# Performance work log

Hardware: AMD Instinct MI355X
Metric: run time of the kernel (lower is better)

Reference implementation:

```python
import jax, jax.numpy as jnp
import numpy as np

NEG = -1e9


def setup_inputs() -> dict:
    key = jax.random.key(0)
    kq, kk, kv, ke = jax.random.split(key, 4)
    B, H, S, D = 4, 16, 2048, 64
    q = jax.random.normal(kq, (B, H, S, D), dtype=jnp.float32)
    k = jax.random.normal(kk, (B, H, S, D), dtype=jnp.float32)
    v = jax.random.normal(kv, (B, H, S, D), dtype=jnp.float32)
    event_length = jax.random.randint(ke, (B,), 0, S, dtype=jnp.int32)
    return {"q": q, "k": k, "v": v, "event_length": event_length}


def reference(q, k, v, event_length):
    B, H, S, D = q.shape
    scale = jnp.sqrt(jnp.asarray(D, dtype=jnp.float32))
    # [b,h,s,q] scores
    scores = jnp.einsum('bhsd,bhqd->bhsq', q, k) / scale
    idx = jnp.arange(S)
    el = event_length[:, None]  # [B,1]
    valid = idx[None, :] < el   # [B,S]
    # mask[b,s,q] = valid[b,s] & valid[b,q]; broadcast over heads
    mask = (valid[:, None, :, None] & valid[:, None, None, :])  # [B,1,S,S]
    scores = jnp.where(mask, scores, NEG)
    attn = jax.nn.softmax(scores, axis=-1)
    # dropout p=0.0 (eval): identity
    out = jnp.einsum('bhsq,bhqd->bhsd', attn, v)
    return out
```

## Files before the change

### kernel.cpp

```cpp
#include <hip/hip_runtime.h>
#include <hip/hip_bf16.h>


#define SQ 2048
#define DH 64
#define NBH 64
#define TK 64
#define NTILE 32
#define TILE_B 8192
#define LDE 72
#define LVP 68

typedef __attribute__((ext_vector_type(4))) float f32x4;
typedef __attribute__((ext_vector_type(8))) short bf16x8;
typedef __attribute__((ext_vector_type(4))) unsigned int u32x4;
typedef __attribute__((ext_vector_type(2))) unsigned int u32x2;

__device__ __forceinline__ unsigned int pk2(float lo, float hi) {
    __hip_bfloat162 h = __float22bfloat162_rn(float2{lo, hi});
    union { __hip_bfloat162 h; unsigned int u; } c; c.h = h;
    return c.u;
}

__device__ __forceinline__ float bfu16_to_f(unsigned short s) {
    union { unsigned int u; float f; } c; c.u = ((unsigned int)s) << 16;
    return c.f;
}

__device__ __forceinline__ void async_cp16(const void* g, void* l) {
    __builtin_amdgcn_global_load_lds(
        (const __attribute__((address_space(1))) unsigned int*)g,
        (__attribute__((address_space(3))) unsigned int*)l, 16, 0, 0);
}


__global__ __launch_bounds__(256)
void convkv(const float* __restrict__ K, const float* __restrict__ V,
            const int* __restrict__ EL, float* __restrict__ MV,
            char* __restrict__ Kbt, char* __restrict__ Vbt) {
    const int bh = blockIdx.x >> 5;
    const int kt = blockIdx.x & 31;
    const int k0 = kt * TK;
    const int el = EL[bh >> 4];
    const int t = threadIdx.x;
    const int r  = t >> 2;
    const int dc = t & 3;

    __shared__ short LV[64][LVP];

    {
        const float* vp = V + ((size_t)bh * SQ + k0 + r) * DH + dc * 16;
        f32x4 a = *(const f32x4*)vp;
        f32x4 b = *(const f32x4*)(vp + 4);
        f32x4 c2 = *(const f32x4*)(vp + 8);
        f32x4 d2 = *(const f32x4*)(vp + 12);
        u32x4 w0, w1;
        w0[0] = pk2(a[0], a[1]);  w0[1] = pk2(a[2], a[3]);
        w0[2] = pk2(b[0], b[1]);  w0[3] = pk2(b[2], b[3]);
        w1[0] = pk2(c2[0], c2[1]); w1[1] = pk2(c2[2], c2[3]);
        w1[2] = pk2(d2[0], d2[1]); w1[3] = pk2(d2[2], d2[3]);
        *(u32x4*)&LV[r][dc * 16]     = w0;
        *(u32x4*)&LV[r][dc * 16 + 8] = w1;
    }

    if (k0 < el) {
        const float* kp = K + ((size_t)bh * SQ + k0 + r) * DH + dc * 16;
        f32x4 a = *(const f32x4*)kp;
        f32x4 b = *(const f32x4*)(kp + 4);
        f32x4 c2 = *(const f32x4*)(kp + 8);
        f32x4 d2 = *(const f32x4*)(kp + 12);
        u32x4 w0, w1;
        w0[0] = pk2(a[0], a[1]);  w0[1] = pk2(a[2], a[3]);
        w0[2] = pk2(b[0], b[1]);  w0[3] = pk2(b[2], b[3]);
        w1[0] = pk2(c2[0], c2[1]); w1[1] = pk2(c2[2], c2[3]);
        w1[2] = pk2(d2[0], d2[1]); w1[3] = pk2(d2[2], d2[3]);
        char* kb = Kbt + (size_t)(bh * NTILE + kt) * TILE_B + r * 128;
        *(u32x4*)(kb + (((dc * 2)     ^ (r & 7)) << 4)) = w0;
        *(u32x4*)(kb + (((dc * 2 + 1) ^ (r & 7)) << 4)) = w1;
    }

    __syncthreads();

    const int dd  = t >> 2;
    const int seg = t & 3;
    float msum = 0.f;
    unsigned int wv[8];
    #pragma unroll
    for (int i = 0; i < 8; ++i) {
        const int pos = seg * 16 + 2 * i;
        const int key = (pos & ~31) | ((pos & 4) << 2) | ((pos & 24) >> 1) | (pos & 3);
        const unsigned short s0 = (unsigned short)LV[key][dd];
        const unsigned short s1 = (unsigned short)LV[key + 1][dd];
        msum += bfu16_to_f(s0) + bfu16_to_f(s1);
        wv[i] = (unsigned int)s0 | ((unsigned int)s1 << 16);
    }
    msum += __shfl_xor(msum, 1);
    msum += __shfl_xor(msum, 2);
    if (seg == 0) atomicAdd(&MV[bh * DH + dd], msum * (1.0f / (float)SQ));

    if (k0 < el) {
        char* vb = Vbt + (size_t)(bh * NTILE + kt) * TILE_B + dd * 128;
        u32x4 o0 = {wv[0], wv[1], wv[2], wv[3]};
        u32x4 o1 = {wv[4], wv[5], wv[6], wv[7]};
        *(u32x4*)(vb + (((seg * 2)     ^ (dd & 7)) << 4)) = o0;
        *(u32x4*)(vb + (((seg * 2 + 1) ^ (dd & 7)) << 4)) = o1;
    }
}

__global__ __launch_bounds__(256, 4)
void flash7(const float* __restrict__ Q, const int* __restrict__ EL,
            const float* __restrict__ MV, float* __restrict__ O,
            const char* __restrict__ Kbt, const char* __restrict__ Vbt,
            int* __restrict__ ticket) {
    const int t = threadIdx.x;

    {
        const int bh0 = blockIdx.x & (NBH - 1);
        const int qb0 = (blockIdx.x >> 6) * 128;
        const int elb = EL[bh0 >> 4];
        if (qb0 >= elb) {
            float* Op = O + (size_t)bh0 * SQ * DH;
            const int c16 = t & 15, r0 = t >> 4;
            f32x4 mv = *(const f32x4*)(MV + bh0 * DH + c16 * 4);
            #pragma unroll
            for (int i = 0; i < 8; ++i)
                *(f32x4*)(Op + (size_t)(qb0 + r0 + i * 16) * DH + c16 * 4) = mv;
        }
    }

    const int el0 = EL[0], el1 = EL[1], el2 = EL[2], el3 = EL[3];
    const int v0 = (el0 + 127) >> 7, v1 = (el1 + 127) >> 7;
    const int v2 = (el2 + 127) >> 7, v3 = (el3 + 127) >> 7;
    const int n0 = 16 * v0, n1 = n0 + 16 * v1, n2 = n1 + 16 * v2;
    const int nvalid = n2 + 16 * v3;

    __shared__ short KT[2][TK * DH];
    __shared__ short VT[2][TK * DH];
    __shared__ int item_s;

    const int wq = t >> 6, lane = t & 63, qd = lane >> 4, c = lane & 15;
    const int cs = c & 7;

    for (;;) {
        if (t == 0) item_s = atomicAdd(ticket, 1);
        __syncthreads();
        const int it = item_s;
        if (it >= nvalid) break;

        int b, u, vb, el;
        if      (it < n0) { b = 0; u = it;      vb = v0; el = el0; }
        else if (it < n1) { b = 1; u = it - n0; vb = v1; el = el1; }
        else if (it < n2) { b = 2; u = it - n1; vb = v2; el = el2; }
        else              { b = 3; u = it - n2; vb = v3; el = el3; }
        const int head  = u / vb;
        const int qt    = u - head * vb;
        const int bh    = b * 16 + head;
        const int qbase = qt * 128;

        const float* Qp = Q + (size_t)bh * SQ * DH;
        float*       Op = O + (size_t)bh * SQ * DH;
        const char*  Kt = Kbt + (size_t)bh * NTILE * TILE_B;
        const char*  Vt = Vbt + (size_t)bh * NTILE * TILE_B;

        const float sc = 0.125f * 1.44269504f;
        bf16x8 qf[2][2];
        #pragma unroll
        for (int nt = 0; nt < 2; ++nt) {
            const int row = qbase + wq * 32 + nt * 16 + c;
            #pragma unroll
            for (int kc = 0; kc < 2; ++kc) {
                const float* p = Qp + (size_t)row * DH + kc * 32 + qd * 8;
                f32x4 a  = *(const f32x4*)p;
                f32x4 bq = *(const f32x4*)(p + 4);
                u32x4 f;
                f[0] = pk2(a[0] * sc, a[1] * sc);
                f[1] = pk2(a[2] * sc, a[3] * sc);
                f[2] = pk2(bq[0] * sc, bq[1] * sc);
                f[3] = pk2(bq[2] * sc, bq[3] * sc);
                qf[nt][kc] = *(bf16x8*)&f;
            }
        }

        float l_[2] = {0.f, 0.f};
        f32x4 oacc[4][2];
        #pragma unroll
        for (int dt = 0; dt < 4; ++dt) {
            oacc[dt][0] = (f32x4){0.f, 0.f, 0.f, 0.f};
            oacc[dt][1] = (f32x4){0.f, 0.f, 0.f, 0.f};
        }

        const int nkt = (el + TK - 1) >> 6;

        {
            async_cp16(Kt + (size_t)t * 16,        (char*)&KT[0][0] + wq * 1024);
            async_cp16(Kt + 4096 + (size_t)t * 16, (char*)&KT[0][0] + 4096 + wq * 1024);
            async_cp16(Vt + (size_t)t * 16,        (char*)&VT[0][0] + wq * 1024);
            async_cp16(Vt + 4096 + (size_t)t * 16, (char*)&VT[0][0] + 4096 + wq * 1024);
        }
        asm volatile("s_waitcnt vmcnt(0)" ::: "memory");
        __syncthreads();

        int buf = 0;
        for (int kt = 0; kt < nkt; ++kt) {
            if (kt + 1 < nkt) {
                const char* gK = Kt + (size_t)(kt + 1) * TILE_B + t * 16;
                const char* gV = Vt + (size_t)(kt + 1) * TILE_B + t * 16;
                char* lK = (char*)&KT[buf ^ 1][0] + wq * 1024;
                char* lV = (char*)&VT[buf ^ 1][0] + wq * 1024;
                async_cp16(gK,        lK);
                async_cp16(gK + 4096, lK + 4096);
                async_cp16(gV,        lV);
                async_cp16(gV + 4096, lV + 4096);
            }
            const int k0 = kt * TK;

            const char* Kb = (const char*)&KT[buf][0];
            f32x4 st[4][2];
            #pragma unroll
            for (int mt = 0; mt < 4; ++mt) {
                const char* rp = Kb + (mt * 16 + c) * 128;
                bf16x8 a0 = *(const bf16x8*)(rp + (((qd)     ^ cs) << 4));
                bf16x8 a1 = *(const bf16x8*)(rp + (((qd + 4) ^ cs) << 4));
                #pragma unroll
                for (int nt = 0; nt < 2; ++nt) {
                    f32x4 acc = (f32x4){0.f, 0.f, 0.f, 0.f};
                    acc = __builtin_amdgcn_mfma_f32_16x16x32_bf16(a0, qf[nt][0], acc, 0, 0, 0);
                    acc = __builtin_amdgcn_mfma_f32_16x16x32_bf16(a1, qf[nt][1], acc, 0, 0, 0);
                    st[mt][nt] = acc;
                }
            }

            if (k0 + TK > el) {
                #pragma unroll
                for (int mt = 0; mt < 4; ++mt)
                    #pragma unroll
                    for (int r = 0; r < 4; ++r)
                        if (k0 + mt * 16 + qd * 4 + r >= el) {
                            st[mt][0][r] = -1e30f;
                            st[mt][1][r] = -1e30f;
                        }
            }

            u32x4 pw[2][2];
            #pragma unroll
            for (int nt = 0; nt < 2; ++nt) {
                #pragma unroll
                for (int mt = 0; mt < 4; ++mt) {
                    const float p0 = __builtin_amdgcn_exp2f(st[mt][nt][0]);
                    const float p1 = __builtin_amdgcn_exp2f(st[mt][nt][1]);
                    const float p2 = __builtin_amdgcn_exp2f(st[mt][nt][2]);
                    const float p3 = __builtin_amdgcn_exp2f(st[mt][nt][3]);
                    l_[nt] += (p0 + p1) + (p2 + p3);
                    pw[nt][mt >> 1][(mt & 1) * 2]     = pk2(p0, p1);
                    pw[nt][mt >> 1][(mt & 1) * 2 + 1] = pk2(p2, p3);
                }
            }

            const char* Vb = (const char*)&VT[buf][0];
            #pragma unroll
            for (int kc = 0; kc < 2; ++kc) {
                bf16x8 pb0 = *(bf16x8*)&pw[0][kc];
                bf16x8 pb1 = *(bf16x8*)&pw[1][kc];
                #pragma unroll
                for (int dt = 0; dt < 4; ++dt) {
                    const char* vp = Vb + (dt * 16 + c) * 128 + (((kc * 4 + qd) ^ cs) << 4);
                    bf16x8 vf = *(const bf16x8*)vp;
                    oacc[dt][0] = __builtin_amdgcn_mfma_f32_16x16x32_bf16(vf, pb0, oacc[dt][0], 0, 0, 0);
                    oacc[dt][1] = __builtin_amdgcn_mfma_f32_16x16x32_bf16(vf, pb1, oacc[dt][1], 0, 0, 0);
                }
            }

            asm volatile("s_waitcnt vmcnt(0)" ::: "memory");
            __syncthreads();
            buf ^= 1;
        }

        #pragma unroll
        for (int nt = 0; nt < 2; ++nt) {
            l_[nt] += __shfl_xor(l_[nt], 16);
            l_[nt] += __shfl_xor(l_[nt], 32);
        }

        #pragma unroll
        for (int nt = 0; nt < 2; ++nt) {
            const int qrow = qbase + wq * 32 + nt * 16 + c;
            if (qrow < el) {
                const float inv = 1.0f / l_[nt];
                #pragma unroll
                for (int dt = 0; dt < 4; ++dt) {
                    f32x4 o = oacc[dt][nt];
                    o[0] *= inv; o[1] *= inv; o[2] *= inv; o[3] *= inv;
                    *(f32x4*)(Op + (size_t)qrow * DH + dt * 16 + qd * 4) = o;
                }
            } else {
                #pragma unroll
                for (int dt = 0; dt < 4; ++dt)
                    *(f32x4*)(Op + (size_t)qrow * DH + dt * 16 + qd * 4) =
                        *(const f32x4*)(MV + bh * DH + dt * 16 + qd * 4);
            }
        }
    }
}


__global__ __launch_bounds__(256)
void meanv_k(const float* __restrict__ V, float* __restrict__ MV) {
    const int bh  = blockIdx.x >> 4;
    const int seg = blockIdx.x & 15;
    const float* vp = V + ((size_t)bh * SQ + (size_t)seg * 128) * DH;
    const int c = threadIdx.x & 15;
    const int r = threadIdx.x >> 4;
    const float* p = vp + (size_t)r * DH + c * 4;
    f32x4 s0 = *(const f32x4*)(p);
    f32x4 s1 = *(const f32x4*)(p + 16 * DH);
    f32x4 s2 = *(const f32x4*)(p + 32 * DH);
    f32x4 s3 = *(const f32x4*)(p + 48 * DH);
    s0 += *(const f32x4*)(p + 64 * DH);
    s1 += *(const f32x4*)(p + 80 * DH);
    s2 += *(const f32x4*)(p + 96 * DH);
    s3 += *(const f32x4*)(p + 112 * DH);
    f32x4 s = (s0 + s1) + (s2 + s3);
    __shared__ f32x4 red[16][16];
    red[r][c] = s;
    __syncthreads();
    if (threadIdx.x < 16) {
        f32x4 a = red[0][threadIdx.x];
        #pragma unroll
        for (int j = 1; j < 16; ++j) a += red[j][threadIdx.x];
        const float inv = 1.0f / (float)SQ;
        atomicAdd(&MV[bh * DH + threadIdx.x * 4 + 0], a[0] * inv);
        atomicAdd(&MV[bh * DH + threadIdx.x * 4 + 1], a[1] * inv);
        atomicAdd(&MV[bh * DH + threadIdx.x * 4 + 2], a[2] * inv);
        atomicAdd(&MV[bh * DH + threadIdx.x * 4 + 3], a[3] * inv);
    }
}

__global__ __launch_bounds__(256, 3)
void flash5(const float* __restrict__ Q, const float* __restrict__ K,
            const float* __restrict__ V, const int* __restrict__ EL,
            const float* __restrict__ MV, float* __restrict__ O,
            int* __restrict__ ticket) {
    const int t = threadIdx.x;
    {
        const int bh0    = blockIdx.x & (NBH - 1);
        const int qbase0 = (blockIdx.x >> 6) * 128;
        const int elb    = EL[bh0 >> 4];
        if (qbase0 >= elb) {
            float* Op = O + (size_t)bh0 * SQ * DH;
            const int c16 = t & 15, r0 = t >> 4;
            f32x4 mv = *(const f32x4*)(MV + bh0 * DH + c16 * 4);
            #pragma unroll
            for (int i = 0; i < 8; ++i)
                *(f32x4*)(Op + (size_t)(qbase0 + r0 + i * 16) * DH + c16 * 4) = mv;
        }
    }

    const int el0 = EL[0], el1 = EL[1], el2 = EL[2], el3 = EL[3];
    const int v0 = (el0 + 127) >> 7, v1 = (el1 + 127) >> 7;
    const int v2 = (el2 + 127) >> 7, v3 = (el3 + 127) >> 7;
    const int n0 = 16 * v0, n1 = n0 + 16 * v1, n2 = n1 + 16 * v2;
    const int nvalid = n2 + 16 * v3;

    __shared__ short Kb[TK][LDE];
    __shared__ short Vt[DH][LDE];
    __shared__ short Pl[4][32][LDE];
    __shared__ int item_s;

    const int wq = t >> 6, lane = t & 63, qd = lane >> 4, c = lane & 15;
    const int ksrow = t >> 2;
    const int ksdc  = t & 3;
    const int vpair = t & 31;
    const int vdg   = t >> 5;

    for (;;) {
        if (t == 0) item_s = atomicAdd(ticket, 1);
        __syncthreads();
        const int it = item_s;
        if (it >= nvalid) break;

        int b, u, vb, el;
        if      (it < n0) { b = 0; u = it;      vb = v0; el = el0; }
        else if (it < n1) { b = 1; u = it - n0; vb = v1; el = el1; }
        else if (it < n2) { b = 2; u = it - n1; vb = v2; el = el2; }
        else              { b = 3; u = it - n2; vb = v3; el = el3; }
        const int head  = u / vb;
        const int qt    = u - head * vb;
        const int bh    = b * 16 + head;
        const int qbase = qt * 128;

        const size_t base = (size_t)bh * SQ * DH;
        const float* Qp = Q + base;
        const float* Kp = K + base;
        const float* Vp = V + base;
        float* Op = O + base;

        const float sc = 0.125f * 1.44269504f;
        bf16x8 qf[2][2];
        #pragma unroll
        for (int nt = 0; nt < 2; ++nt) {
            const int row = qbase + wq * 32 + nt * 16 + c;
            #pragma unroll
            for (int kc = 0; kc < 2; ++kc) {
                const float* p = Qp + (size_t)row * DH + kc * 32 + qd * 8;
                f32x4 a  = *(const f32x4*)p;
                f32x4 bb = *(const f32x4*)(p + 4);
                u32x4 f;
                f[0] = pk2(a[0] * sc, a[1] * sc);
                f[1] = pk2(a[2] * sc, a[3] * sc);
                f[2] = pk2(bb[0] * sc, bb[1] * sc);
                f[3] = pk2(bb[2] * sc, bb[3] * sc);
                qf[nt][kc] = *(bf16x8*)&f;
            }
        }

        float l_[2] = {0.f, 0.f};
        f32x4 oacc[4][2];
        #pragma unroll
        for (int dt = 0; dt < 4; ++dt)
            #pragma unroll
            for (int nt = 0; nt < 2; ++nt)
                oacc[dt][nt] = (f32x4){0.f, 0.f, 0.f, 0.f};

        const int nkt = (el + TK - 1) / TK;

        f32x4 kg0, kg1, kg2, kg3, vg0, vg1, vg2, vg3;
        {
            const float* kp = Kp + (size_t)ksrow * DH + ksdc * 16;
            kg0 = *(const f32x4*)kp;
            kg1 = *(const f32x4*)(kp + 4);
            kg2 = *(const f32x4*)(kp + 8);
            kg3 = *(const f32x4*)(kp + 12);
            const float* vp0 = Vp + (size_t)(2 * vpair) * DH + vdg * 8;
            vg0 = *(const f32x4*)vp0;
            vg1 = *(const f32x4*)(vp0 + 4);
            vg2 = *(const f32x4*)(vp0 + DH);
            vg3 = *(const f32x4*)(vp0 + DH + 4);
        }

        for (int kt = 0; kt < nkt; ++kt) {
            const int k0 = kt * TK;

            __syncthreads();
            {
                u32x4 w0, w1;
                w0[0] = pk2(kg0[0], kg0[1]); w0[1] = pk2(kg0[2], kg0[3]);
                w0[2] = pk2(kg1[0], kg1[1]); w0[3] = pk2(kg1[2], kg1[3]);
                w1[0] = pk2(kg2[0], kg2[1]); w1[1] = pk2(kg2[2], kg2[3]);
                w1[2] = pk2(kg3[0], kg3[1]); w1[3] = pk2(kg3[2], kg3[3]);
                *(u32x4*)&Kb[ksrow][ksdc * 16]     = w0;
                *(u32x4*)&Kb[ksrow][ksdc * 16 + 8] = w1;
            }
            {
                #pragma unroll
                for (int i = 0; i < 4; ++i) {
                    *(unsigned int*)&Vt[vdg * 8 + i][2 * vpair]     = pk2(vg0[i], vg2[i]);
                    *(unsigned int*)&Vt[vdg * 8 + 4 + i][2 * vpair] = pk2(vg1[i], vg3[i]);
                }
            }
            __syncthreads();

            if (kt + 1 < nkt) {
                const int kn = k0 + TK;
                const float* kp = Kp + (size_t)(kn + ksrow) * DH + ksdc * 16;
                kg0 = *(const f32x4*)kp;
                kg1 = *(const f32x4*)(kp + 4);
                kg2 = *(const f32x4*)(kp + 8);
                kg3 = *(const f32x4*)(kp + 12);
                const float* vp0 = Vp + (size_t)(kn + 2 * vpair) * DH + vdg * 8;
                vg0 = *(const f32x4*)vp0;
                vg1 = *(const f32x4*)(vp0 + 4);
                vg2 = *(const f32x4*)(vp0 + DH);
                vg3 = *(const f32x4*)(vp0 + DH + 4);
            }

            f32x4 st[4][2];
            #pragma unroll
            for (int mt = 0; mt < 4; ++mt) {
                bf16x8 a0 = *(const bf16x8*)&Kb[mt * 16 + c][qd * 8];
                bf16x8 a1 = *(const bf16x8*)&Kb[mt * 16 + c][32 + qd * 8];
                #pragma unroll
                for (int nt = 0; nt < 2; ++nt) {
                    f32x4 acc = (f32x4){0.f, 0.f, 0.f, 0.f};
                    acc = __builtin_amdgcn_mfma_f32_16x16x32_bf16(a0, qf[nt][0], acc, 0, 0, 0);
                    acc = __builtin_amdgcn_mfma_f32_16x16x32_bf16(a1, qf[nt][1], acc, 0, 0, 0);
                    st[mt][nt] = acc;
                }
            }

            if (k0 + TK > el) {
                #pragma unroll
                for (int mt = 0; mt < 4; ++mt)
                    #pragma unroll
                    for (int r = 0; r < 4; ++r)
                        if (k0 + mt * 16 + qd * 4 + r >= el) {
                            st[mt][0][r] = -1e30f;
                            st[mt][1][r] = -1e30f;
                        }
            }

            #pragma unroll
            for (int nt = 0; nt < 2; ++nt) {
                #pragma unroll
                for (int mt = 0; mt < 4; ++mt) {
                    const float p0 = exp2f(st[mt][nt][0]);
                    const float p1 = exp2f(st[mt][nt][1]);
                    const float p2 = exp2f(st[mt][nt][2]);
                    const float p3 = exp2f(st[mt][nt][3]);
                    l_[nt] += (p0 + p1) + (p2 + p3);
                    u32x2 pw;
                    pw[0] = pk2(p0, p1);
                    pw[1] = pk2(p2, p3);
                    *(u32x2*)&Pl[wq][nt * 16 + c][mt * 16 + qd * 4] = pw;
                }
            }

            #pragma unroll
            for (int kc = 0; kc < 2; ++kc) {
                bf16x8 pb0 = *(const bf16x8*)&Pl[wq][c][kc * 32 + qd * 8];
                bf16x8 pb1 = *(const bf16x8*)&Pl[wq][16 + c][kc * 32 + qd * 8];
                #pragma unroll
                for (int dt = 0; dt < 4; ++dt) {
                    bf16x8 vf = *(const bf16x8*)&Vt[dt * 16 + c][kc * 32 + qd * 8];
                    oacc[dt][0] = __builtin_amdgcn_mfma_f32_16x16x32_bf16(vf, pb0, oacc[dt][0], 0, 0, 0);
                    oacc[dt][1] = __builtin_amdgcn_mfma_f32_16x16x32_bf16(vf, pb1, oacc[dt][1], 0, 0, 0);
                }
            }
        }

        #pragma unroll
        for (int nt = 0; nt < 2; ++nt) {
            l_[nt] += __shfl_xor(l_[nt], 16);
            l_[nt] += __shfl_xor(l_[nt], 32);
        }

        #pragma unroll
        for (int nt = 0; nt < 2; ++nt) {
            const int row = qbase + wq * 32 + nt * 16 + c;
            if (row < el) {
                const float inv = 1.0f / l_[nt];
                #pragma unroll
                for (int dt = 0; dt < 4; ++dt) {
                    f32x4 o = oacc[dt][nt];
                    o[0] *= inv; o[1] *= inv; o[2] *= inv; o[3] *= inv;
                    *(f32x4*)(Op + (size_t)row * DH + dt * 16 + qd * 4) = o;
                }
            } else {
                #pragma unroll
                for (int dt = 0; dt < 4; ++dt) {
                    f32x4 mv = *(const f32x4*)(MV + bh * DH + dt * 16 + qd * 4);
                    *(f32x4*)(Op + (size_t)row * DH + dt * 16 + qd * 4) = mv;
                }
            }
        }
    }
}


extern "C" void kernel_launch(void* const* d_in, const int* in_sizes, int n_in,
                              void* d_out, int out_size, void* d_ws, size_t ws_size,
                              hipStream_t stream) {
    const float* q  = (const float*)d_in[0];
    const float* k  = (const float*)d_in[1];
    const float* v  = (const float*)d_in[2];
    const int*   el = (const int*)d_in[3];
    float* out = (float*)d_out;

    const size_t kbt_bytes = (size_t)NBH * NTILE * TILE_B;
    const size_t needed    = 65536 + 2 * kbt_bytes;

    if (ws_size >= needed) {
        float* mv  = (float*)d_ws;
        int*   tk  = (int*)((char*)d_ws + 16384);
        char*  kbt = (char*)d_ws + 65536;
        char*  vbt = kbt + kbt_bytes;

        hipMemsetAsync(d_ws, 0, 65536, stream);
        convkv<<<dim3(NBH * NTILE), dim3(256), 0, stream>>>(k, v, el, mv, kbt, vbt);
        flash7<<<dim3(NBH * (SQ / 128)), dim3(256), 0, stream>>>(q, el, mv, out, kbt, vbt, tk);
    } else {
        float* mv = (float*)d_ws;
        int*   tk = (int*)((char*)d_ws + NBH * DH * sizeof(float));

        hipMemsetAsync(d_ws, 0, NBH * DH * sizeof(float) + 64, stream);
        meanv_k<<<dim3(NBH * 16), dim3(256), 0, stream>>>(v, mv);
        flash5<<<dim3(NBH * (SQ / 128)), dim3(256), 0, stream>>>(q, k, v, el, mv, out, tk);
    }
}
```

Baseline: 197.2 us.

## Load K/V fragments directly from global in MFMA order, per-wave work items

The convkv pass now writes K and V tiles in an MFMA-fragment-ordered layout, so each lane reads its operands straight from global memory with coalesced 16-byte loads. The double-buffered LDS staging and block-wide barriers in the attention kernel are removed. Work items become 32-row chunks claimed per wave through a per-wave atomic ticket, and occupancy is lowered to 3 blocks per CU to make room for the extra registers holding K/V fragments. The trade is more L2/global traffic, with no LDS sharing across waves and no explicit prefetch, in exchange for finer load balancing and no synchronisation.

New measurement: 210.4 us. 6.7% more time.

```diff
diff --git a/kernel.cpp b/kernel.cpp
--- a/kernel.cpp
+++ b/kernel.cpp
@@ -25,12 +25,6 @@
 __device__ __forceinline__ float bfu16_to_f(unsigned short s) {
     union { unsigned int u; float f; } c; c.u = ((unsigned int)s) << 16;
     return c.f;
-}
-
-__device__ __forceinline__ void async_cp16(const void* g, void* l) {
-    __builtin_amdgcn_global_load_lds(
-        (const __attribute__((address_space(1))) unsigned int*)g,
-        (__attribute__((address_space(3))) unsigned int*)l, 16, 0, 0);
 }
 
 
@@ -74,9 +68,12 @@
         w0[2] = pk2(b[0], b[1]);  w0[3] = pk2(b[2], b[3]);
         w1[0] = pk2(c2[0], c2[1]); w1[1] = pk2(c2[2], c2[3]);
         w1[2] = pk2(d2[0], d2[1]); w1[3] = pk2(d2[2], d2[3]);
-        char* kb = Kbt + (size_t)(bh * NTILE + kt) * TILE_B + r * 128;
-        *(u32x4*)(kb + (((dc * 2)     ^ (r & 7)) << 4)) = w0;
-        *(u32x4*)(kb + (((dc * 2 + 1) ^ (r & 7)) << 4)) = w1;
+        char* kb = Kbt + (size_t)(bh * NTILE + kt) * TILE_B;
+        const int fi  = (r >> 4) * 2 + (dc >> 1);
+        const int qd0 = (dc & 1) * 2;
+        char* d0 = kb + fi * 1024 + qd0 * 256 + (r & 15) * 16;
+        *(u32x4*)d0         = w0;
+        *(u32x4*)(d0 + 256) = w1;
     }
 
     __syncthreads();
@@ -99,16 +96,19 @@
     if (seg == 0) atomicAdd(&MV[bh * DH + dd], msum * (1.0f / (float)SQ));
 
     if (k0 < el) {
-        char* vb = Vbt + (size_t)(bh * NTILE + kt) * TILE_B + dd * 128;
+        char* vbb = Vbt + (size_t)(bh * NTILE + kt) * TILE_B;
+        const int fi  = (seg >> 1) * 4 + (dd >> 4);
+        const int qd0 = (seg & 1) * 2;
+        char* d0 = vbb + fi * 1024 + qd0 * 256 + (dd & 15) * 16;
         u32x4 o0 = {wv[0], wv[1], wv[2], wv[3]};
         u32x4 o1 = {wv[4], wv[5], wv[6], wv[7]};
-        *(u32x4*)(vb + (((seg * 2)     ^ (dd & 7)) << 4)) = o0;
-        *(u32x4*)(vb + (((seg * 2 + 1) ^ (dd & 7)) << 4)) = o1;
-    }
-}
-
-__global__ __launch_bounds__(256, 4)
-void flash7(const float* __restrict__ Q, const int* __restrict__ EL,
+        *(u32x4*)d0         = o0;
+        *(u32x4*)(d0 + 256) = o1;
+    }
+}
+
+__global__ __launch_bounds__(256, 3)
+void flash8(const float* __restrict__ Q, const int* __restrict__ EL,
             const float* __restrict__ MV, float* __restrict__ O,
             const char* __restrict__ Kbt, const char* __restrict__ Vbt,
             int* __restrict__ ticket) {
@@ -117,56 +117,55 @@
     {
         const int bh0 = blockIdx.x & (NBH - 1);
         const int qb0 = (blockIdx.x >> 6) * 128;
-        const int elb = EL[bh0 >> 4];
-        if (qb0 >= elb) {
+        const int el32b = (EL[bh0 >> 4] + 31) & ~31;
+        if (qb0 + 127 >= el32b) {
             float* Op = O + (size_t)bh0 * SQ * DH;
             const int c16 = t & 15, r0 = t >> 4;
             f32x4 mv = *(const f32x4*)(MV + bh0 * DH + c16 * 4);
             #pragma unroll
-            for (int i = 0; i < 8; ++i)
-                *(f32x4*)(Op + (size_t)(qb0 + r0 + i * 16) * DH + c16 * 4) = mv;
+            for (int i = 0; i < 8; ++i) {
+                const int row = qb0 + r0 + i * 16;
+                if (row >= el32b)
+                    *(f32x4*)(Op + (size_t)row * DH + c16 * 4) = mv;
+            }
         }
     }
 
     const int el0 = EL[0], el1 = EL[1], el2 = EL[2], el3 = EL[3];
-    const int v0 = (el0 + 127) >> 7, v1 = (el1 + 127) >> 7;
-    const int v2 = (el2 + 127) >> 7, v3 = (el3 + 127) >> 7;
-    const int n0 = 16 * v0, n1 = n0 + 16 * v1, n2 = n1 + 16 * v2;
-    const int nvalid = n2 + 16 * v3;
-
-    __shared__ short KT[2][TK * DH];
-    __shared__ short VT[2][TK * DH];
-    __shared__ int item_s;
-
-    const int wq = t >> 6, lane = t & 63, qd = lane >> 4, c = lane & 15;
-    const int cs = c & 7;
+    const int w0_ = (el0 + 31) >> 5, w1_ = (el1 + 31) >> 5;
+    const int w2_ = (el2 + 31) >> 5, w3_ = (el3 + 31) >> 5;
+    const int n0 = 16 * w0_, n1 = n0 + 16 * w1_, n2 = n1 + 16 * w2_;
+    const int nvalid = n2 + 16 * w3_;
+
+    const int lane = t & 63, qd = lane >> 4, c = lane & 15;
+    const float sc = 0.125f * 1.44269504f;
 
     for (;;) {
-        if (t == 0) item_s = atomicAdd(ticket, 1);
-        __syncthreads();
-        const int it = item_s;
+        int mytk = 0;
+        if (lane == 0) mytk = atomicAdd(ticket, 1);
+        const int it = __shfl(mytk, 0);
         if (it >= nvalid) break;
 
-        int b, u, vb, el;
-        if      (it < n0) { b = 0; u = it;      vb = v0; el = el0; }
-        else if (it < n1) { b = 1; u = it - n0; vb = v1; el = el1; }
-        else if (it < n2) { b = 2; u = it - n1; vb = v2; el = el2; }
-        else              { b = 3; u = it - n2; vb = v3; el = el3; }
-        const int head  = u / vb;
-        const int qt    = u - head * vb;
+        int b, u, wb, el;
+        if      (it < n0) { b = 0; u = it;      wb = w0_; el = el0; }
+        else if (it < n1) { b = 1; u = it - n0; wb = w1_; el = el1; }
+        else if (it < n2) { b = 2; u = it - n1; wb = w2_; el = el2; }
+        else              { b = 3; u = it - n2; wb = w3_; el = el3; }
+        const int head  = u / wb;
+        const int qt    = u - head * wb;
         const int bh    = b * 16 + head;
-        const int qbase = qt * 128;
+        const int qbase = qt * 32;
 
         const float* Qp = Q + (size_t)bh * SQ * DH;
         float*       Op = O + (size_t)bh * SQ * DH;
-        const char*  Kt = Kbt + (size_t)bh * NTILE * TILE_B;
-        const char*  Vt = Vbt + (size_t)bh * NTILE * TILE_B;
-
-        const float sc = 0.125f * 1.44269504f;
+        const size_t tb = (size_t)bh * NTILE * TILE_B + (size_t)lane * 16;
+        const char*  Kt = Kbt + tb;
+        const char*  Vt = Vbt + tb;
+
         bf16x8 qf[2][2];
         #pragma unroll
         for (int nt = 0; nt < 2; ++nt) {
-            const int row = qbase + wq * 32 + nt * 16 + c;
+            const int row = qbase + nt * 16 + c;
             #pragma unroll
             for (int kc = 0; kc < 2; ++kc) {
                 const float* p = Qp + (size_t)row * DH + kc * 32 + qd * 8;
@@ -191,88 +190,65 @@
 
         const int nkt = (el + TK - 1) >> 6;
 
-        {
-            async_cp16(Kt + (size_t)t * 16,        (char*)&KT[0][0] + wq * 1024);
-            async_cp16(Kt + 4096 + (size_t)t * 16, (char*)&KT[0][0] + 4096 + wq * 1024);
-            async_cp16(Vt + (size_t)t * 16,        (char*)&VT[0][0] + wq * 1024);
-            async_cp16(Vt + 4096 + (size_t)t * 16, (char*)&VT[0][0] + 4096 + wq * 1024);
-        }
-        asm volatile("s_waitcnt vmcnt(0)" ::: "memory");
-        __syncthreads();
-
-        int buf = 0;
         for (int kt = 0; kt < nkt; ++kt) {
-            if (kt + 1 < nkt) {
-                const char* gK = Kt + (size_t)(kt + 1) * TILE_B + t * 16;
-                const char* gV = Vt + (size_t)(kt + 1) * TILE_B + t * 16;
-                char* lK = (char*)&KT[buf ^ 1][0] + wq * 1024;
-                char* lV = (char*)&VT[buf ^ 1][0] + wq * 1024;
-                async_cp16(gK,        lK);
-                async_cp16(gK + 4096, lK + 4096);
-                async_cp16(gV,        lV);
-                async_cp16(gV + 4096, lV + 4096);
-            }
+            const char* kb = Kt + (size_t)kt * TILE_B;
+            const char* vb = Vt + (size_t)kt * TILE_B;
+
+            bf16x8 ka[8];
+            #pragma unroll
+            for (int i = 0; i < 8; ++i)
+                ka[i] = *(const bf16x8*)(kb + i * 1024);
+            bf16x8 va[8];
+            #pragma unroll
+            for (int i = 0; i < 8; ++i)
+                va[i] = *(const bf16x8*)(vb + i * 1024);
+
             const int k0 = kt * TK;
-
-            const char* Kb = (const char*)&KT[buf][0];
-            f32x4 st[4][2];
+            const bool straddle = (k0 + TK > el);
+
+            u32x4 pw[2][2];
             #pragma unroll
             for (int mt = 0; mt < 4; ++mt) {
-                const char* rp = Kb + (mt * 16 + c) * 128;
-                bf16x8 a0 = *(const bf16x8*)(rp + (((qd)     ^ cs) << 4));
-                bf16x8 a1 = *(const bf16x8*)(rp + (((qd + 4) ^ cs) << 4));
-                #pragma unroll
-                for (int nt = 0; nt < 2; ++nt) {
-                    f32x4 acc = (f32x4){0.f, 0.f, 0.f, 0.f};
-                    acc = __builtin_amdgcn_mfma_f32_16x16x32_bf16(a0, qf[nt][0], acc, 0, 0, 0);
-                    acc = __builtin_amdgcn_mfma_f32_16x16x32_bf16(a1, qf[nt][1], acc, 0, 0, 0);
-                    st[mt][nt] = acc;
-                }
-            }
-
-            if (k0 + TK > el) {
-                #pragma unroll
-                for (int mt = 0; mt < 4; ++mt)
+                f32x4 s0 = (f32x4){0.f, 0.f, 0.f, 0.f};
+                s0 = __builtin_amdgcn_mfma_f32_16x16x32_bf16(ka[mt*2],   qf[0][0], s0, 0, 0, 0);
+                s0 = __builtin_amdgcn_mfma_f32_16x16x32_bf16(ka[mt*2+1], qf[0][1], s0, 0, 0, 0);
+                f32x4 s1 = (f32x4){0.f, 0.f, 0.f, 0.f};
+                s1 = __builtin_amdgcn_mfma_f32_16x16x32_bf16(ka[mt*2],   qf[1][0], s1, 0, 0, 0);
+                s1 = __builtin_amdgcn_mfma_f32_16x16x32_bf16(ka[mt*2+1], qf[1][1], s1, 0, 0, 0);
+
+                if (straddle) {
                     #pragma unroll
                     for (int r = 0; r < 4; ++r)
                         if (k0 + mt * 16 + qd * 4 + r >= el) {
-                            st[mt][0][r] = -1e30f;
-                            st[mt][1][r] = -1e30f;
+                            s0[r] = -1e30f;
+                            s1[r] = -1e30f;
                         }
-            }
-
-            u32x4 pw[2][2];
-            #pragma unroll
-            for (int nt = 0; nt < 2; ++nt) {
-                #pragma unroll
-                for (int mt = 0; mt < 4; ++mt) {
-                    const float p0 = __builtin_amdgcn_exp2f(st[mt][nt][0]);
-                    const float p1 = __builtin_amdgcn_exp2f(st[mt][nt][1]);
-                    const float p2 = __builtin_amdgcn_exp2f(st[mt][nt][2]);
-                    const float p3 = __builtin_amdgcn_exp2f(st[mt][nt][3]);
+                }
+
+                #pragma unroll
+                for (int nt = 0; nt < 2; ++nt) {
+                    const f32x4 s = nt ? s1 : s0;
+                    const float p0 = __builtin_amdgcn_exp2f(s[0]);
+                    const float p1 = __builtin_amdgcn_exp2f(s[1]);
+                    const float p2 = __builtin_amdgcn_exp2f(s[2]);
+                    const float p3 = __builtin_amdgcn_exp2f(s[3]);
                     l_[nt] += (p0 + p1) + (p2 + p3);
                     pw[nt][mt >> 1][(mt & 1) * 2]     = pk2(p0, p1);
                     pw[nt][mt >> 1][(mt & 1) * 2 + 1] = pk2(p2, p3);
                 }
             }
 
-            const char* Vb = (const char*)&VT[buf][0];
             #pragma unroll
             for (int kc = 0; kc < 2; ++kc) {
                 bf16x8 pb0 = *(bf16x8*)&pw[0][kc];
                 bf16x8 pb1 = *(bf16x8*)&pw[1][kc];
                 #pragma unroll
                 for (int dt = 0; dt < 4; ++dt) {
-                    const char* vp = Vb + (dt * 16 + c) * 128 + (((kc * 4 + qd) ^ cs) << 4);
-                    bf16x8 vf = *(const bf16x8*)vp;
+                    bf16x8 vf = va[kc * 4 + dt];
                     oacc[dt][0] = __builtin_amdgcn_mfma_f32_16x16x32_bf16(vf, pb0, oacc[dt][0], 0, 0, 0);
                     oacc[dt][1] = __builtin_amdgcn_mfma_f32_16x16x32_bf16(vf, pb1, oacc[dt][1], 0, 0, 0);
                 }
             }
-
-            asm volatile("s_waitcnt vmcnt(0)" ::: "memory");
-            __syncthreads();
-            buf ^= 1;
         }
 
         #pragma unroll
@@ -283,7 +259,7 @@
 
         #pragma unroll
         for (int nt = 0; nt < 2; ++nt) {
-            const int qrow = qbase + wq * 32 + nt * 16 + c;
+            const int qrow = qbase + nt * 16 + c;
             if (qrow < el) {
                 const float inv = 1.0f / l_[nt];
                 #pragma unroll
@@ -576,7 +552,7 @@
 
         hipMemsetAsync(d_ws, 0, 65536, stream);
         convkv<<<dim3(NBH * NTILE), dim3(256), 0, stream>>>(k, v, el, mv, kbt, vbt);
-        flash7<<<dim3(NBH * (SQ / 128)), dim3(256), 0, stream>>>(q, el, mv, out, kbt, vbt, tk);
+        flash8<<<dim3(NBH * (SQ / 128)), dim3(256), 0, stream>>>(q, el, mv, out, kbt, vbt, tk);
     } else {
         float* mv = (float*)d_ws;
         int*   tk = (int*)((char*)d_ws + NBH * DH * sizeof(float));
```

## Triple-buffer K/V tiles, enlarge query blocks, pre-swizzle fragment layout

Applied to the files above, without the earlier changes.

The attention kernel now runs 512-thread blocks that each cover 256 query rows, so every staged K/V tile feeds twice as much work. K/V tiles are prefetched two steps ahead through a three-slot LDS ring, with partial vmcnt waits replacing the full drain at the end of each step. The conversion kernel writes K/V in an MFMA-fragment-ordered layout so LDS reads become plain contiguous lane loads with no XOR swizzle. Work items are split into eight ticket groups with batches sorted by length, and s_setprio is raised around the MFMA sections. LDS use per block grows and the early-exit mean fill loop changes shape, so occupancy and correctness of the fill path are the main risks.

Measured after the change: 193.8 us. No clear change (-1.7%).

```diff
diff --git a/kernel.cpp b/kernel.cpp
--- a/kernel.cpp
+++ b/kernel.cpp
@@ -15,6 +15,8 @@
 typedef __attribute__((ext_vector_type(8))) short bf16x8;
 typedef __attribute__((ext_vector_type(4))) unsigned int u32x4;
 typedef __attribute__((ext_vector_type(2))) unsigned int u32x2;
+
+#define VMCNT(n) asm volatile("s_waitcnt vmcnt(" #n ")" ::: "memory")
 
 __device__ __forceinline__ unsigned int pk2(float lo, float hi) {
     __hip_bfloat162 h = __float22bfloat162_rn(float2{lo, hi});
@@ -74,9 +76,12 @@
         w0[2] = pk2(b[0], b[1]);  w0[3] = pk2(b[2], b[3]);
         w1[0] = pk2(c2[0], c2[1]); w1[1] = pk2(c2[2], c2[3]);
         w1[2] = pk2(d2[0], d2[1]); w1[3] = pk2(d2[2], d2[3]);
-        char* kb = Kbt + (size_t)(bh * NTILE + kt) * TILE_B + r * 128;
-        *(u32x4*)(kb + (((dc * 2)     ^ (r & 7)) << 4)) = w0;
-        *(u32x4*)(kb + (((dc * 2 + 1) ^ (r & 7)) << 4)) = w1;
+        char* kb = Kbt + (size_t)(bh * NTILE + kt) * TILE_B;
+        const int fi  = (r >> 4) * 2 + (dc >> 1);
+        const int qd0 = (dc & 1) * 2;
+        char* d0 = kb + fi * 1024 + qd0 * 256 + (r & 15) * 16;
+        *(u32x4*)d0         = w0;
+        *(u32x4*)(d0 + 256) = w1;
     }
 
     __syncthreads();
@@ -99,24 +104,27 @@
     if (seg == 0) atomicAdd(&MV[bh * DH + dd], msum * (1.0f / (float)SQ));
 
     if (k0 < el) {
-        char* vb = Vbt + (size_t)(bh * NTILE + kt) * TILE_B + dd * 128;
+        char* vbb = Vbt + (size_t)(bh * NTILE + kt) * TILE_B;
+        const int fi  = (seg >> 1) * 4 + (dd >> 4);
+        const int qd0 = (seg & 1) * 2;
+        char* d0 = vbb + fi * 1024 + qd0 * 256 + (dd & 15) * 16;
         u32x4 o0 = {wv[0], wv[1], wv[2], wv[3]};
         u32x4 o1 = {wv[4], wv[5], wv[6], wv[7]};
-        *(u32x4*)(vb + (((seg * 2)     ^ (dd & 7)) << 4)) = o0;
-        *(u32x4*)(vb + (((seg * 2 + 1) ^ (dd & 7)) << 4)) = o1;
-    }
-}
-
-__global__ __launch_bounds__(256, 4)
-void flash7(const float* __restrict__ Q, const int* __restrict__ EL,
-            const float* __restrict__ MV, float* __restrict__ O,
-            const char* __restrict__ Kbt, const char* __restrict__ Vbt,
-            int* __restrict__ ticket) {
+        *(u32x4*)d0         = o0;
+        *(u32x4*)(d0 + 256) = o1;
+    }
+}
+
+__global__ __launch_bounds__(512, 4)
+void flash10(const float* __restrict__ Q, const int* __restrict__ EL,
+             const float* __restrict__ MV, float* __restrict__ O,
+             const char* __restrict__ Kbt, const char* __restrict__ Vbt,
+             int* __restrict__ ticket) {
     const int t = threadIdx.x;
 
     {
         const int bh0 = blockIdx.x & (NBH - 1);
-        const int qb0 = (blockIdx.x >> 6) * 128;
+        const int qb0 = (blockIdx.x >> 6) * 256;
         const int elb = EL[bh0 >> 4];
         if (qb0 >= elb) {
             float* Op = O + (size_t)bh0 * SQ * DH;
@@ -124,45 +132,67 @@
             f32x4 mv = *(const f32x4*)(MV + bh0 * DH + c16 * 4);
             #pragma unroll
             for (int i = 0; i < 8; ++i)
-                *(f32x4*)(Op + (size_t)(qb0 + r0 + i * 16) * DH + c16 * 4) = mv;
-        }
-    }
-
-    const int el0 = EL[0], el1 = EL[1], el2 = EL[2], el3 = EL[3];
-    const int v0 = (el0 + 127) >> 7, v1 = (el1 + 127) >> 7;
-    const int v2 = (el2 + 127) >> 7, v3 = (el3 + 127) >> 7;
-    const int n0 = 16 * v0, n1 = n0 + 16 * v1, n2 = n1 + 16 * v2;
-    const int nvalid = n2 + 16 * v3;
-
-    __shared__ short KT[2][TK * DH];
-    __shared__ short VT[2][TK * DH];
+                *(f32x4*)(Op + (size_t)(qb0 + r0 + i * 32) * DH + c16 * 4) = mv;
+        }
+    }
+
+    int ka0 = EL[0], va0 = 0;
+    int ka1 = EL[1], va1 = 1;
+    int ka2 = EL[2], va2 = 2;
+    int ka3 = EL[3], va3 = 3;
+    #define CSWAP(x, y) if (ka##x < ka##y) { int tk_ = ka##x, tv_ = va##x; \
+        ka##x = ka##y; va##x = va##y; ka##y = tk_; va##y = tv_; }
+    CSWAP(0, 1) CSWAP(2, 3) CSWAP(0, 2) CSWAP(1, 3) CSWAP(1, 2)
+    #undef CSWAP
+    const int c0 = 2 * ((ka0 + 255) >> 8);
+    const int c1 = 2 * ((ka1 + 255) >> 8);
+    const int c2 = 2 * ((ka2 + 255) >> 8);
+    const int c3 = 2 * ((ka3 + 255) >> 8);
+    const int nvalid = c0 + c1 + c2 + c3;
+
+    __shared__ char KB[3 * TILE_B];
+    __shared__ char VB[3 * TILE_B];
     __shared__ int item_s;
 
+    const int grp = blockIdx.x & 7;
     const int wq = t >> 6, lane = t & 63, qd = lane >> 4, c = lane & 15;
-    const int cs = c & 7;
+    const float sc = 0.125f * 1.44269504f;
 
     for (;;) {
-        if (t == 0) item_s = atomicAdd(ticket, 1);
+        if (t == 0) item_s = atomicAdd(&ticket[grp], 1);
         __syncthreads();
         const int it = item_s;
         if (it >= nvalid) break;
 
-        int b, u, vb, el;
-        if      (it < n0) { b = 0; u = it;      vb = v0; el = el0; }
-        else if (it < n1) { b = 1; u = it - n0; vb = v1; el = el1; }
-        else if (it < n2) { b = 2; u = it - n1; vb = v2; el = el2; }
-        else              { b = 3; u = it - n2; vb = v3; el = el3; }
-        const int head  = u / vb;
-        const int qt    = u - head * vb;
-        const int bh    = b * 16 + head;
-        const int qbase = qt * 128;
+        int u = it, b, el;
+        if (u < c0)             { b = va0; el = ka0; }
+        else { u -= c0;
+        if (u < c1)             { b = va1; el = ka1; }
+        else { u -= c1;
+        if (u < c2)             { b = va2; el = ka2; }
+        else { u -= c2;           b = va3; el = ka3; } } }
+        const int vb_ = (el + 255) >> 8;
+        const int hh  = u / vb_;
+        const int qt  = u - hh * vb_;
+        const int bh  = b * 16 + grp + hh * 8;
+        const int qbase = qt * 256;
 
         const float* Qp = Q + (size_t)bh * SQ * DH;
         float*       Op = O + (size_t)bh * SQ * DH;
-        const char*  Kt = Kbt + (size_t)bh * NTILE * TILE_B;
-        const char*  Vt = Vbt + (size_t)bh * NTILE * TILE_B;
-
-        const float sc = 0.125f * 1.44269504f;
+        const char*  Kt = Kbt + (size_t)bh * NTILE * TILE_B + t * 16;
+        const char*  Vt = Vbt + (size_t)bh * NTILE * TILE_B + t * 16;
+        char* const  kdst = KB + wq * 1024;
+        char* const  vdst = VB + wq * 1024;
+
+        const int nkt = (el + TK - 1) >> 6;
+
+        async_cp16(Kt, kdst);
+        async_cp16(Vt, vdst);
+        if (nkt > 1) {
+            async_cp16(Kt + TILE_B, kdst + TILE_B);
+            async_cp16(Vt + TILE_B, vdst + TILE_B);
+        }
+
         bf16x8 qf[2][2];
         #pragma unroll
         for (int nt = 0; nt < 2; ++nt) {
@@ -189,38 +219,29 @@
             oacc[dt][1] = (f32x4){0.f, 0.f, 0.f, 0.f};
         }
 
-        const int nkt = (el + TK - 1) >> 6;
-
-        {
-            async_cp16(Kt + (size_t)t * 16,        (char*)&KT[0][0] + wq * 1024);
-            async_cp16(Kt + 4096 + (size_t)t * 16, (char*)&KT[0][0] + 4096 + wq * 1024);
-            async_cp16(Vt + (size_t)t * 16,        (char*)&VT[0][0] + wq * 1024);
-            async_cp16(Vt + 4096 + (size_t)t * 16, (char*)&VT[0][0] + 4096 + wq * 1024);
-        }
-        asm volatile("s_waitcnt vmcnt(0)" ::: "memory");
-        __syncthreads();
-
-        int buf = 0;
         for (int kt = 0; kt < nkt; ++kt) {
-            if (kt + 1 < nkt) {
-                const char* gK = Kt + (size_t)(kt + 1) * TILE_B + t * 16;
-                const char* gV = Vt + (size_t)(kt + 1) * TILE_B + t * 16;
-                char* lK = (char*)&KT[buf ^ 1][0] + wq * 1024;
-                char* lV = (char*)&VT[buf ^ 1][0] + wq * 1024;
-                async_cp16(gK,        lK);
-                async_cp16(gK + 4096, lK + 4096);
-                async_cp16(gV,        lV);
-                async_cp16(gV + 4096, lV + 4096);
-            }
-            const int k0 = kt * TK;
-
-            const char* Kb = (const char*)&KT[buf][0];
+            const int s = kt % 3;
+
+            __syncthreads();
+            if (kt + 2 < nkt) {
+                const int s2 = (kt + 2) % 3;
+                async_cp16(Kt + (size_t)(kt + 2) * TILE_B, kdst + s2 * TILE_B);
+                async_cp16(Vt + (size_t)(kt + 2) * TILE_B, vdst + s2 * TILE_B);
+            }
+            if      (kt + 2 < nkt) VMCNT(4);
+            else if (kt + 1 < nkt) VMCNT(2);
+            else                   VMCNT(0);
+            __syncthreads();
+
+            const char* Kb = KB + s * TILE_B + lane * 16;
+            const char* Vb = VB + s * TILE_B + lane * 16;
+
             f32x4 st[4][2];
+            __builtin_amdgcn_s_setprio(1);
             #pragma unroll
             for (int mt = 0; mt < 4; ++mt) {
-                const char* rp = Kb + (mt * 16 + c) * 128;
-                bf16x8 a0 = *(const bf16x8*)(rp + (((qd)     ^ cs) << 4));
-                bf16x8 a1 = *(const bf16x8*)(rp + (((qd + 4) ^ cs) << 4));
+                bf16x8 a0 = *(const bf16x8*)(Kb + (mt * 2) * 1024);
+                bf16x8 a1 = *(const bf16x8*)(Kb + (mt * 2 + 1) * 1024);
                 #pragma unroll
                 for (int nt = 0; nt < 2; ++nt) {
                     f32x4 acc = (f32x4){0.f, 0.f, 0.f, 0.f};
@@ -229,7 +250,9 @@
                     st[mt][nt] = acc;
                 }
             }
-
+            __builtin_amdgcn_s_setprio(0);
+
+            const int k0 = kt * TK;
             if (k0 + TK > el) {
                 #pragma unroll
                 for (int mt = 0; mt < 4; ++mt)
@@ -256,23 +279,19 @@
                 }
             }
 
-            const char* Vb = (const char*)&VT[buf][0];
+            __builtin_amdgcn_s_setprio(1);
             #pragma unroll
             for (int kc = 0; kc < 2; ++kc) {
                 bf16x8 pb0 = *(bf16x8*)&pw[0][kc];
                 bf16x8 pb1 = *(bf16x8*)&pw[1][kc];
                 #pragma unroll
                 for (int dt = 0; dt < 4; ++dt) {
-                    const char* vp = Vb + (dt * 16 + c) * 128 + (((kc * 4 + qd) ^ cs) << 4);
-                    bf16x8 vf = *(const bf16x8*)vp;
+                    bf16x8 vf = *(const bf16x8*)(Vb + (kc * 4 + dt) * 1024);
                     oacc[dt][0] = __builtin_amdgcn_mfma_f32_16x16x32_bf16(vf, pb0, oacc[dt][0], 0, 0, 0);
                     oacc[dt][1] = __builtin_amdgcn_mfma_f32_16x16x32_bf16(vf, pb1, oacc[dt][1], 0, 0, 0);
                 }
             }
-
-            asm volatile("s_waitcnt vmcnt(0)" ::: "memory");
-            __syncthreads();
-            buf ^= 1;
+            __builtin_amdgcn_s_setprio(0);
         }
 
         #pragma unroll
@@ -576,7 +595,7 @@
 
         hipMemsetAsync(d_ws, 0, 65536, stream);
         convkv<<<dim3(NBH * NTILE), dim3(256), 0, stream>>>(k, v, el, mv, kbt, vbt);
-        flash7<<<dim3(NBH * (SQ / 128)), dim3(256), 0, stream>>>(q, el, mv, out, kbt, vbt, tk);
+        flash10<<<dim3(NBH * (SQ / 256)), dim3(512), 0, stream>>>(q, el, mv, out, kbt, vbt, tk);
     } else {
         float* mv = (float*)d_ws;
         int*   tk = (int*)((char*)d_ws + NBH * DH * sizeof(float));
```
